# Performance work log

Measured on AMD Instinct MI355X. Metric: run time of the kernel, lower is better.

The kernel has to match this reference:

```python
import jax, jax.numpy as jnp
import numpy as np

B = 8192
EMBED = 4  # self-attention embed dim


def setup_inputs() -> dict:
    key = jax.random.key(0)
    ks = jax.random.split(key, 20)
    f32 = jnp.float32
    return {
        "inputs": jax.random.normal(ks[0], (B, 8), dtype=f32),
        # MLP chain params (stored as [in, out]; y = x @ W + b)
        "W_fm": jax.random.normal(ks[1], (8, 16), dtype=f32) * 0.1,
        "b_fm": jnp.zeros((16,), dtype=f32),
        "W_c1": jax.random.normal(ks[2], (16, 16), dtype=f32) * 0.1,
        "b_c1": jnp.zeros((16,), dtype=f32),
        "W_p1": jax.random.normal(ks[3], (16, 12), dtype=f32) * 0.1,
        "b_p1": jnp.zeros((12,), dtype=f32),
        "W_c2": jax.random.normal(ks[4], (12, 8), dtype=f32) * 0.1,
        "b_c2": jnp.zeros((8,), dtype=f32),
        "W_p2": jax.random.normal(ks[5], (8, 4), dtype=f32) * 0.1,
        "b_p2": jnp.zeros((4,), dtype=f32),
        "W_c3": jax.random.normal(ks[6], (4, 4), dtype=f32) * 0.1,
        "b_c3": jnp.zeros((4,), dtype=f32),
        # self-attention params
        "rot": jax.random.normal(ks[7], (EMBED, EMBED), dtype=f32),
        "ent": jax.random.normal(ks[8], (EMBED, EMBED), dtype=f32),
        # ConvFilter: 2x2 conv kernel flattened (cross-correlation over 2x2 patch)
        "conv_w": jax.random.normal(ks[9], (4,), dtype=f32) * 0.5,
        "conv_b": jnp.zeros((1,), dtype=f32),
        # head: Linear(1,1)
        "head_w": jax.random.normal(ks[10], (1, 1), dtype=f32),
        "head_b": jnp.zeros((1,), dtype=f32),
    }


def reference(inputs, W_fm, b_fm, W_c1, b_c1, W_p1, b_p1, W_c2, b_c2,
              W_p2, b_p2, W_c3, b_c3, rot, ent, conv_w, conv_b,
              head_w, head_b):
    threshold = 0.0
    shift = 0.0
    # MLP chain: Linear + Tanh blocks
    x = jnp.tanh(inputs @ W_fm + b_fm)   # [B,16]
    x = jnp.tanh(x @ W_c1 + b_c1)        # [B,16]
    x = jnp.tanh(x @ W_p1 + b_p1)        # [B,12]
    x = jnp.tanh(x @ W_c2 + b_c2)        # [B,8]
    x = jnp.tanh(x @ W_p2 + b_p2)        # [B,4]
    x = jnp.tanh(x @ W_c3 + b_c3)        # [B,4]
    # self-attention over the batch axis (as in the original torch.mm)
    q = x @ rot                           # [B,4]
    k = x @ ent                           # [B,4]
    scores = jax.nn.softmax((q @ k.T) / jnp.sqrt(jnp.float32(EMBED)), axis=-1)  # [B,B]
    x = scores @ x                        # [B,4]
    # batched 2x2 conv filter: each sample's 4-vector reshaped to 2x2, one
    # valid conv output -> sum(w * patch) + b; mean of single elem is itself
    filtered = jax.nn.sigmoid(x @ conv_w + conv_b - threshold)[:, None]  # [B,1]
    logits = filtered @ head_w + head_b   # [B,1]
    return jax.nn.sigmoid(logits + shift)
```

## Files before the change

### kernel.cpp

```cpp
#include <hip/hip_runtime.h>
#include <math.h>

#define BATCH 8192
#define BLK 256


template <int IN, int OUT>
__device__ __forceinline__ void layer_tanh(const float* a, float* out,
                                           const float* __restrict__ W,
                                           const float* __restrict__ bias) {
  float acc[OUT];
#pragma unroll
  for (int o = 0; o < OUT; o++) acc[o] = bias[o];
#pragma unroll
  for (int i = 0; i < IN; i++) {
    float ai = a[i];
#pragma unroll
    for (int o = 0; o < OUT; o++) acc[o] = fmaf(ai, W[i * OUT + o], acc[o]);
  }
#pragma unroll
  for (int o = 0; o < OUT; o++) out[o] = tanhf(acc[o]);
}

__global__ __launch_bounds__(BLK) void mlp_kernel(
    const float* __restrict__ in,
    const float* __restrict__ W_fm, const float* __restrict__ b_fm,
    const float* __restrict__ W_c1, const float* __restrict__ b_c1,
    const float* __restrict__ W_p1, const float* __restrict__ b_p1,
    const float* __restrict__ W_c2, const float* __restrict__ b_c2,
    const float* __restrict__ W_p2, const float* __restrict__ b_p2,
    const float* __restrict__ W_c3, const float* __restrict__ b_c3,
    const float* __restrict__ rot, const float* __restrict__ ent,
    float4* __restrict__ xv, float4* __restrict__ qv, float4* __restrict__ kv) {
  __shared__ float w[812];
  const int t = threadIdx.x;
  auto cp = [&](const float* src, int off, int n) {
    for (int i = t; i < n; i += BLK) w[off + i] = src[i];
  };
  cp(W_fm, 0, 128);  cp(b_fm, 128, 16);
  cp(W_c1, 144, 256); cp(b_c1, 400, 16);
  cp(W_p1, 416, 192); cp(b_p1, 608, 12);
  cp(W_c2, 620, 96);  cp(b_c2, 716, 8);
  cp(W_p2, 724, 32);  cp(b_p2, 756, 4);
  cp(W_c3, 760, 16);  cp(b_c3, 776, 4);
  cp(rot, 780, 16);   cp(ent, 796, 16);
  __syncthreads();

  const int r = blockIdx.x * BLK + t;
  const float4* in4 = (const float4*)in;
  float4 i0 = in4[r * 2 + 0];
  float4 i1 = in4[r * 2 + 1];
  float a[16], b[16];
  a[0] = i0.x; a[1] = i0.y; a[2] = i0.z; a[3] = i0.w;
  a[4] = i1.x; a[5] = i1.y; a[6] = i1.z; a[7] = i1.w;

  layer_tanh<8, 16>(a, b, w + 0, w + 128);
  layer_tanh<16, 16>(b, a, w + 144, w + 400);
  layer_tanh<16, 12>(a, b, w + 416, w + 608);
  layer_tanh<12, 8>(b, a, w + 620, w + 716);
  layer_tanh<8, 4>(a, b, w + 724, w + 756);
  layer_tanh<4, 4>(b, a, w + 760, w + 776);
  float q[4], k[4];
#pragma unroll
  for (int d = 0; d < 4; d++) {
    q[d] = a[0] * w[780 + 0 * 4 + d] + a[1] * w[780 + 1 * 4 + d] +
           a[2] * w[780 + 2 * 4 + d] + a[3] * w[780 + 3 * 4 + d];
    k[d] = a[0] * w[796 + 0 * 4 + d] + a[1] * w[796 + 1 * 4 + d] +
           a[2] * w[796 + 2 * 4 + d] + a[3] * w[796 + 3 * 4 + d];
  }
  xv[r] = make_float4(a[0], a[1], a[2], a[3]);
  qv[r] = make_float4(q[0] * 0.5f, q[1] * 0.5f, q[2] * 0.5f, q[3] * 0.5f);
  kv[r] = make_float4(k[0], k[1], k[2], k[3]);
}

__device__ __forceinline__ float dot4(float4 a, float4 b) {
  return fmaf(a.x, b.x, fmaf(a.y, b.y, fmaf(a.z, b.z, a.w * b.w)));
}

template <int CHUNK>
__global__ __launch_bounds__(BLK) void attn_partial(
    const float4* __restrict__ xv, const float4* __restrict__ qv,
    const float4* __restrict__ kv, float* __restrict__ m_arr,
    float* __restrict__ l_arr, float4* __restrict__ o_arr) {
  __shared__ float4 Ks[CHUNK];
  __shared__ float4 Vs[CHUNK];
  const int t = threadIdx.x;
  const int qi = blockIdx.x * BLK + t;
  const int c0 = blockIdx.y * CHUNK;
  for (int i = t; i < CHUNK; i += BLK) {
    Ks[i] = kv[c0 + i];
    Vs[i] = xv[c0 + i];
  }
  __syncthreads();
  const float4 q = qv[qi];

  float m0 = -3.0e38f, m1 = -3.0e38f;
#pragma unroll 4
  for (int j = 0; j < CHUNK; j += 2) {
    float s0 = dot4(q, Ks[j]);
    float s1 = dot4(q, Ks[j + 1]);
    m0 = fmaxf(m0, s0);
    m1 = fmaxf(m1, s1);
  }
  const float m = fmaxf(m0, m1);

  float l0 = 0.f, l1 = 0.f;
  float4 o0 = make_float4(0.f, 0.f, 0.f, 0.f);
  float4 o1 = make_float4(0.f, 0.f, 0.f, 0.f);
#pragma unroll 4
  for (int j = 0; j < CHUNK; j += 2) {
    float4 ka = Ks[j], kb = Ks[j + 1];
    float4 va = Vs[j], vb = Vs[j + 1];
    float s0 = dot4(q, ka);
    float s1 = dot4(q, kb);
    float p0 = __expf(s0 - m);
    float p1 = __expf(s1 - m);
    l0 += p0;
    l1 += p1;
    o0.x = fmaf(p0, va.x, o0.x); o0.y = fmaf(p0, va.y, o0.y);
    o0.z = fmaf(p0, va.z, o0.z); o0.w = fmaf(p0, va.w, o0.w);
    o1.x = fmaf(p1, vb.x, o1.x); o1.y = fmaf(p1, vb.y, o1.y);
    o1.z = fmaf(p1, vb.z, o1.z); o1.w = fmaf(p1, vb.w, o1.w);
  }
  const int idx = blockIdx.y * BATCH + qi;
  m_arr[idx] = m;
  l_arr[idx] = l0 + l1;
  o_arr[idx] = make_float4(o0.x + o1.x, o0.y + o1.y, o0.z + o1.z, o0.w + o1.w);
}

__global__ __launch_bounds__(BLK) void combine_kernel(
    const float* __restrict__ m_arr, const float* __restrict__ l_arr,
    const float4* __restrict__ o_arr, int nsplit,
    const float* __restrict__ conv_w, const float* __restrict__ conv_b,
    const float* __restrict__ head_w, const float* __restrict__ head_b,
    float* __restrict__ out) {
  const int qi = blockIdx.x * BLK + threadIdx.x;
  float m = -3.0e38f;
  for (int s = 0; s < nsplit; s++) m = fmaxf(m, m_arr[s * BATCH + qi]);
  float l = 0.f;
  float4 o = make_float4(0.f, 0.f, 0.f, 0.f);
  for (int s = 0; s < nsplit; s++) {
    float wgt = __expf(m_arr[s * BATCH + qi] - m);
    l = fmaf(l_arr[s * BATCH + qi], wgt, l);
    float4 os = o_arr[s * BATCH + qi];
    o.x = fmaf(os.x, wgt, o.x); o.y = fmaf(os.y, wgt, o.y);
    o.z = fmaf(os.z, wgt, o.z); o.w = fmaf(os.w, wgt, o.w);
  }
  const float inv = 1.0f / l;
  float z = o.x * inv * conv_w[0] + o.y * inv * conv_w[1] +
            o.z * inv * conv_w[2] + o.w * inv * conv_w[3] + conv_b[0];
  float filtered = 1.0f / (1.0f + __expf(-z));
  float logit = fmaf(filtered, head_w[0], head_b[0]);
  out[qi] = 1.0f / (1.0f + __expf(-logit));
}

extern "C" void kernel_launch(void* const* d_in, const int* in_sizes, int n_in,
                              void* d_out, int out_size, void* d_ws,
                              size_t ws_size, hipStream_t stream) {
  const float* in   = (const float*)d_in[0];
  const float* W_fm = (const float*)d_in[1];
  const float* b_fm = (const float*)d_in[2];
  const float* W_c1 = (const float*)d_in[3];
  const float* b_c1 = (const float*)d_in[4];
  const float* W_p1 = (const float*)d_in[5];
  const float* b_p1 = (const float*)d_in[6];
  const float* W_c2 = (const float*)d_in[7];
  const float* b_c2 = (const float*)d_in[8];
  const float* W_p2 = (const float*)d_in[9];
  const float* b_p2 = (const float*)d_in[10];
  const float* W_c3 = (const float*)d_in[11];
  const float* b_c3 = (const float*)d_in[12];
  const float* rot  = (const float*)d_in[13];
  const float* ent  = (const float*)d_in[14];
  const float* conv_w = (const float*)d_in[15];
  const float* conv_b = (const float*)d_in[16];
  const float* head_w = (const float*)d_in[17];
  const float* head_b = (const float*)d_in[18];
  float* out = (float*)d_out;

  char* ws = (char*)d_ws;
  float4* xv = (float4*)(ws + 0);
  float4* qv = (float4*)(ws + 131072);
  float4* kv = (float4*)(ws + 262144);
  char* part = ws + 393216;

  int nsplit;
  if (ws_size >= (size_t)(393216 + 32 * BATCH * 24))
    nsplit = 32;
  else
    nsplit = 8;

  float* m_arr = (float*)part;
  float* l_arr = (float*)(part + (size_t)nsplit * BATCH * 4);
  float4* o_arr = (float4*)(part + (size_t)nsplit * BATCH * 8);

  mlp_kernel<<<BATCH / BLK, BLK, 0, stream>>>(
      in, W_fm, b_fm, W_c1, b_c1, W_p1, b_p1, W_c2, b_c2, W_p2, b_p2, W_c3,
      b_c3, rot, ent, xv, qv, kv);

  dim3 grid(BATCH / BLK, nsplit);
  if (nsplit == 32) {
    attn_partial<256><<<grid, BLK, 0, stream>>>(xv, qv, kv, m_arr, l_arr, o_arr);
  } else {
    attn_partial<1024><<<grid, BLK, 0, stream>>>(xv, qv, kv, m_arr, l_arr, o_arr);
  }

  combine_kernel<<<BATCH / BLK, BLK, 0, stream>>>(
      m_arr, l_arr, o_arr, nsplit, conv_w, conv_b, head_w, head_b, out);
}
```

Baseline: 148.2 us.

## Drop softmax max pass using bounded scores, interleave K/V in global memory

Removes the running-max pass from the split attention, relying on scores staying bounded (tanh outputs times small rotation matrices) so exp does not overflow. This halves the dot products per chunk and lets the combine step sum partials without rescaling. K and V are interleaved into a single array and read directly from global/L2 instead of being staged through shared memory, so the block-level barrier goes away. The split count is fixed at 32. The risk is numerical overflow if score magnitudes were ever large, and the fixed workspace layout no longer checks ws_size.

```diff
diff --git a/kernel.cpp b/kernel.cpp
--- a/kernel.cpp
+++ b/kernel.cpp
@@ -3,6 +3,8 @@
 
 #define BATCH 8192
 #define BLK 256
+#define NSPLIT 32
+#define CHUNK (BATCH / NSPLIT)
 
 
 template <int IN, int OUT>
@@ -31,7 +33,7 @@
     const float* __restrict__ W_p2, const float* __restrict__ b_p2,
     const float* __restrict__ W_c3, const float* __restrict__ b_c3,
     const float* __restrict__ rot, const float* __restrict__ ent,
-    float4* __restrict__ xv, float4* __restrict__ qv, float4* __restrict__ kv) {
+    float4* __restrict__ qv, float4* __restrict__ kvx) {
   __shared__ float w[812];
   const int t = threadIdx.x;
   auto cp = [&](const float* src, int off, int n) {
@@ -68,53 +70,36 @@
     k[d] = a[0] * w[796 + 0 * 4 + d] + a[1] * w[796 + 1 * 4 + d] +
            a[2] * w[796 + 2 * 4 + d] + a[3] * w[796 + 3 * 4 + d];
   }
-  xv[r] = make_float4(a[0], a[1], a[2], a[3]);
   qv[r] = make_float4(q[0] * 0.5f, q[1] * 0.5f, q[2] * 0.5f, q[3] * 0.5f);
-  kv[r] = make_float4(k[0], k[1], k[2], k[3]);
+  kvx[2 * r + 0] = make_float4(k[0], k[1], k[2], k[3]);
+  kvx[2 * r + 1] = make_float4(a[0], a[1], a[2], a[3]);
 }
 
 __device__ __forceinline__ float dot4(float4 a, float4 b) {
   return fmaf(a.x, b.x, fmaf(a.y, b.y, fmaf(a.z, b.z, a.w * b.w)));
 }
 
-template <int CHUNK>
 __global__ __launch_bounds__(BLK) void attn_partial(
-    const float4* __restrict__ xv, const float4* __restrict__ qv,
-    const float4* __restrict__ kv, float* __restrict__ m_arr,
+    const float4* __restrict__ kvx, const float4* __restrict__ qv,
     float* __restrict__ l_arr, float4* __restrict__ o_arr) {
-  __shared__ float4 Ks[CHUNK];
-  __shared__ float4 Vs[CHUNK];
   const int t = threadIdx.x;
   const int qi = blockIdx.x * BLK + t;
   const int c0 = blockIdx.y * CHUNK;
-  for (int i = t; i < CHUNK; i += BLK) {
-    Ks[i] = kv[c0 + i];
-    Vs[i] = xv[c0 + i];
-  }
-  __syncthreads();
   const float4 q = qv[qi];
-
-  float m0 = -3.0e38f, m1 = -3.0e38f;
-#pragma unroll 4
-  for (int j = 0; j < CHUNK; j += 2) {
-    float s0 = dot4(q, Ks[j]);
-    float s1 = dot4(q, Ks[j + 1]);
-    m0 = fmaxf(m0, s0);
-    m1 = fmaxf(m1, s1);
-  }
-  const float m = fmaxf(m0, m1);
 
   float l0 = 0.f, l1 = 0.f;
   float4 o0 = make_float4(0.f, 0.f, 0.f, 0.f);
   float4 o1 = make_float4(0.f, 0.f, 0.f, 0.f);
 #pragma unroll 4
   for (int j = 0; j < CHUNK; j += 2) {
-    float4 ka = Ks[j], kb = Ks[j + 1];
-    float4 va = Vs[j], vb = Vs[j + 1];
+    const float4 ka = kvx[(c0 + j) * 2 + 0];
+    const float4 va = kvx[(c0 + j) * 2 + 1];
+    const float4 kb = kvx[(c0 + j) * 2 + 2];
+    const float4 vb = kvx[(c0 + j) * 2 + 3];
     float s0 = dot4(q, ka);
     float s1 = dot4(q, kb);
-    float p0 = __expf(s0 - m);
-    float p1 = __expf(s1 - m);
+    float p0 = __expf(s0);
+    float p1 = __expf(s1);
     l0 += p0;
     l1 += p1;
     o0.x = fmaf(p0, va.x, o0.x); o0.y = fmaf(p0, va.y, o0.y);
@@ -123,28 +108,23 @@
     o1.z = fmaf(p1, vb.z, o1.z); o1.w = fmaf(p1, vb.w, o1.w);
   }
   const int idx = blockIdx.y * BATCH + qi;
-  m_arr[idx] = m;
   l_arr[idx] = l0 + l1;
   o_arr[idx] = make_float4(o0.x + o1.x, o0.y + o1.y, o0.z + o1.z, o0.w + o1.w);
 }
 
 __global__ __launch_bounds__(BLK) void combine_kernel(
-    const float* __restrict__ m_arr, const float* __restrict__ l_arr,
-    const float4* __restrict__ o_arr, int nsplit,
+    const float* __restrict__ l_arr, const float4* __restrict__ o_arr,
     const float* __restrict__ conv_w, const float* __restrict__ conv_b,
     const float* __restrict__ head_w, const float* __restrict__ head_b,
     float* __restrict__ out) {
   const int qi = blockIdx.x * BLK + threadIdx.x;
-  float m = -3.0e38f;
-  for (int s = 0; s < nsplit; s++) m = fmaxf(m, m_arr[s * BATCH + qi]);
   float l = 0.f;
   float4 o = make_float4(0.f, 0.f, 0.f, 0.f);
-  for (int s = 0; s < nsplit; s++) {
-    float wgt = __expf(m_arr[s * BATCH + qi] - m);
-    l = fmaf(l_arr[s * BATCH + qi], wgt, l);
+#pragma unroll
+  for (int s = 0; s < NSPLIT; s++) {
+    l += l_arr[s * BATCH + qi];
     float4 os = o_arr[s * BATCH + qi];
-    o.x = fmaf(os.x, wgt, o.x); o.y = fmaf(os.y, wgt, o.y);
-    o.z = fmaf(os.z, wgt, o.z); o.w = fmaf(os.w, wgt, o.w);
+    o.x += os.x; o.y += os.y; o.z += os.z; o.w += os.w;
   }
   const float inv = 1.0f / l;
   float z = o.x * inv * conv_w[0] + o.y * inv * conv_w[1] +
@@ -179,32 +159,18 @@
   float* out = (float*)d_out;
 
   char* ws = (char*)d_ws;
-  float4* xv = (float4*)(ws + 0);
-  float4* qv = (float4*)(ws + 131072);
-  float4* kv = (float4*)(ws + 262144);
-  char* part = ws + 393216;
-
-  int nsplit;
-  if (ws_size >= (size_t)(393216 + 32 * BATCH * 24))
-    nsplit = 32;
-  else
-    nsplit = 8;
-
-  float* m_arr = (float*)part;
-  float* l_arr = (float*)(part + (size_t)nsplit * BATCH * 4);
-  float4* o_arr = (float4*)(part + (size_t)nsplit * BATCH * 8);
+  float4* qv  = (float4*)(ws + 0);
+  float4* kvx = (float4*)(ws + (128 << 10));
+  float*  l_arr = (float*)(ws + (384 << 10));
+  float4* o_arr = (float4*)(ws + (384 << 10) + NSPLIT * BATCH * 4);
 
   mlp_kernel<<<BATCH / BLK, BLK, 0, stream>>>(
       in, W_fm, b_fm, W_c1, b_c1, W_p1, b_p1, W_c2, b_c2, W_p2, b_p2, W_c3,
-      b_c3, rot, ent, xv, qv, kv);
+      b_c3, rot, ent, qv, kvx);
 
-  dim3 grid(BATCH / BLK, nsplit);
-  if (nsplit == 32) {
-    attn_partial<256><<<grid, BLK, 0, stream>>>(xv, qv, kv, m_arr, l_arr, o_arr);
-  } else {
-    attn_partial<1024><<<grid, BLK, 0, stream>>>(xv, qv, kv, m_arr, l_arr, o_arr);
-  }
+  dim3 grid(BATCH / BLK, NSPLIT);
+  attn_partial<<<grid, BLK, 0, stream>>>(kvx, qv, l_arr, o_arr);
 
   combine_kernel<<<BATCH / BLK, BLK, 0, stream>>>(
-      m_arr, l_arr, o_arr, nsplit, conv_w, conv_b, head_w, head_b, out);
+      l_arr, o_arr, conv_w, conv_b, head_w, head_b, out);
 }
```

Measured after the change: 130.7 us. 1.13x faster.
